# Kernel tuning notes

Hardware: AMD Instinct MI355X
Metric: run time of the kernel (lower is better)

Reference implementation:

```python
import jax, jax.numpy as jnp
import numpy as np

# config constants
D = 1024       # main_dim
HD = 64        # attn_head_dim
NH = 16        # attention heads = D // HD
H = 16         # main_head_num (routing heads)
KH = 8         # main_key_head_num
KC = 2         # main_key_repeat_num (KH*KC == H)
N = 128        # block_size
E = 4096       # total_layer_expert_num
RE = 4         # aux_router_expert_num
DE = 4         # selected experts per router
ET = RE * DE   # 16
B, S = 1, 2048
T = B * S
BC = T // N    # 16
EPS = 1e-5
THETA = 10000.0


def rmsnorm(x, w):
    return x * jax.lax.rsqrt(jnp.mean(x * x, axis=-1, keepdims=True) + EPS) * w


def l2norm(x):
    n = jnp.sqrt(jnp.sum(x * x, axis=-1, keepdims=True))
    return x / jnp.maximum(n, EPS)


def rope(x):
    # x: (b, h, s, a); matches RotaryEmb: y1 = x1*cos + x2*sin, y2 = -x1*sin + x2*cos
    a = x.shape[-1]
    s = x.shape[2]
    inv_freq = (1.0 / THETA) ** (jnp.arange(0, a, 2, dtype=jnp.float32) / a)
    freqs = jnp.arange(s, dtype=jnp.float32)[:, None] * inv_freq[None, :]  # (s, a/2)
    cos, sin = jnp.cos(freqs), jnp.sin(freqs)
    x1, x2 = jnp.split(x, 2, axis=-1)
    return jnp.concatenate([x1 * cos + x2 * sin, -x1 * sin + x2 * cos], axis=-1)


def setup_inputs() -> dict:
    key = jax.random.key(0)
    ks = jax.random.split(key, 10)
    return {
        "x_input": jax.random.normal(ks[0], (B, S, D), jnp.float32),
        "indices": jax.random.randint(ks[1], (BC, RE, DE), 0, E),
        "scores": jax.random.normal(ks[2], (T, ET, H), jnp.float32),
        "attn_w": jax.random.normal(ks[3], (D, 3 * D), jnp.float32) * 0.02,
        "attn_out_w": jax.random.normal(ks[4], (D, D), jnp.float32) * 0.02,
        "attn_norm_w": jnp.ones((D,), jnp.float32),
        "ffn_norm_w": jnp.ones((D,), jnp.float32),
        "ffn_experts": jax.random.normal(ks[5], (3, E, D, 1), jnp.float32) * 0.02,
        "keys": jax.random.normal(ks[6], (KH, D, E), jnp.float32) * 0.02,
        "head_probs": jnp.full((1, RE, E, H), 1.0 / H, jnp.float32)
                      + 0.01 * jax.random.normal(ks[7], (1, RE, E, H), jnp.float32),
        "score_probs": jnp.full((2, 1, RE, E, H), 0.5, jnp.float32)
                       + 0.01 * jax.random.normal(ks[8], (2, 1, RE, E, H), jnp.float32),
    }


def reference(x_input, indices, scores, attn_w, attn_out_w, attn_norm_w,
              ffn_norm_w, ffn_experts, keys, head_probs, score_probs):
    # --- attention block ---
    x = rmsnorm(x_input, attn_norm_w)
    qkv = x @ attn_w                                   # (b, s, 3d)
    xq, xk, xv = jnp.split(qkv, 3, axis=-1)

    def heads(t):  # 'b s (h a) -> b h s a'
        return t.reshape(B, S, NH, HD).transpose(0, 2, 1, 3)

    xq, xk, xv = heads(xq), heads(xk), heads(xv)
    xq, xk = l2norm(xq), l2norm(xk)                    # qk_norm
    xq, xk = rope(xq), rope(xk)

    att = jnp.einsum('bhqa,bhka->bhqk', xq, xk) / np.sqrt(HD)
    causal = jnp.tril(jnp.ones((S, S), bool))
    att = jnp.where(causal, att, -jnp.inf)
    att = jax.nn.softmax(att, axis=-1)
    x_attn = jnp.einsum('bhqk,bhka->bhqa', att, xv)
    x_attn = x_attn.transpose(0, 2, 1, 3).reshape(B, S, D)
    x_attn_output = x_attn @ attn_out_w
    x_ffn_input = x_attn_output + x_input

    # --- product-key routing ---
    x_ffn = rmsnorm(x_ffn_input, ffn_norm_w)
    xf = x_ffn.reshape(T, D)

    keys_r = jnp.repeat(keys, KC, axis=0)              # (H, D, E)
    ms = jnp.einsum('td,hde->teh', xf, keys_r)         # (T, E, H)

    idx_flat = indices.reshape(BC, ET)                 # (BC, ET)
    idx_tok = jnp.repeat(idx_flat, N, axis=0)          # (T, ET), token t -> block t//N
    main_g = jnp.take_along_axis(ms, idx_tok[:, :, None], axis=1)  # (T, ET, H)

    r_idx = jnp.arange(RE)[None, :, None]
    sp = score_probs[:, 0]                             # (2, RE, E, H)
    sp_g = sp[:, r_idx, indices]                       # (2, BC, RE, DE, H)
    sp_g = jnp.repeat(sp_g.reshape(2, BC, ET, H), N, axis=1)       # (2, T, ET, H)

    comb = jax.nn.sigmoid(sp_g[0] * main_g + sp_g[1] * scores)     # (T, ET, H)

    hp_g = head_probs[0][r_idx, indices]               # (BC, RE, DE, H)
    hp_g = jnp.repeat(hp_g.reshape(BC, ET, H), N, axis=0)          # (T, ET, H)

    w = jnp.sum(comb * hp_g, axis=-1)                  # (T, ET) pair weights

    # --- grouped GEMM over tiny (d -> expert_dim -> d) experts, SwiGLU ---
    Wg = ffn_experts[:, idx_tok]                       # (3, T, ET, D, expert_dim)
    h0 = jnp.einsum('td,tedk->tek', xf, Wg[0])
    h1 = jnp.einsum('td,tedk->tek', xf, Wg[1])
    act = jax.nn.silu(h0) * h1 * w[:, :, None]         # (T, ET, expert_dim)
    out = jnp.einsum('tek,tedk->td', act, Wg[2])       # sum over selected experts

    return out.reshape(B, S, D) + x_ffn_input
```

## Files before the change

### kernel.cpp

```cpp
#include <hip/hip_runtime.h>
#include <hip/hip_bf16.h>
#include <math.h>

#define D_   1024
#define HD_  64
#define NH_  16
#define H_   16
#define KH_  8
#define NT_  128
#define E_   4096
#define RE_  4
#define DE_  4
#define ET_  16
#define S_   2048
#define T_   2048
#define BC_  16
#define EPS_ 1e-5f

typedef short s16x8 __attribute__((ext_vector_type(8)));
typedef float f32x4 __attribute__((ext_vector_type(4)));

__device__ __forceinline__ unsigned short f2bf(float f) {
    union { float f; unsigned int u; } v; v.f = f;
    unsigned int r = (v.u + 0x7fffu + ((v.u >> 16) & 1u)) >> 16;
    return (unsigned short)r;
}
__device__ __forceinline__ float bf2f(unsigned short u) {
    union { unsigned int i; float f; } v;
    v.i = ((unsigned int)u) << 16;
    return v.f;
}

#define GLOAD16(gp, lp) __builtin_amdgcn_global_load_lds(                      \
    (__attribute__((address_space(1))) void*)(gp),                             \
    (__attribute__((address_space(3))) void*)(lp), 16, 0, 0)

__global__ __launch_bounds__(256) void rmsnorm_bf16_kernel(
    const float* __restrict__ x, const float* __restrict__ w,
    unsigned short* __restrict__ out)
{
    int row = blockIdx.x, tid = threadIdx.x;
    __shared__ float sred[4];
    float4 v = ((const float4*)(x + (size_t)row * D_))[tid];
    float ss = v.x*v.x + v.y*v.y + v.z*v.z + v.w*v.w;
#pragma unroll
    for (int off = 32; off > 0; off >>= 1) ss += __shfl_xor(ss, off);
    if ((tid & 63) == 0) sred[tid >> 6] = ss;
    __syncthreads();
    float tot = sred[0] + sred[1] + sred[2] + sred[3];
    float scale = rsqrtf(tot * (1.0f / D_) + EPS_);
    float4 wv = ((const float4*)w)[tid];
    ushort4 o;
    o.x = f2bf(v.x * scale * wv.x);
    o.y = f2bf(v.y * scale * wv.y);
    o.z = f2bf(v.z * scale * wv.z);
    o.w = f2bf(v.w * scale * wv.w);
    *(ushort4*)(out + (size_t)row * D_ + tid * 4) = o;
}

__global__ __launch_bounds__(256) void rmsnorm_dual_kernel(
    const float* __restrict__ x, const float* __restrict__ w,
    float* __restrict__ out, unsigned short* __restrict__ outb)
{
    int row = blockIdx.x, tid = threadIdx.x;
    __shared__ float sred[4];
    float4 v = ((const float4*)(x + (size_t)row * D_))[tid];
    float ss = v.x*v.x + v.y*v.y + v.z*v.z + v.w*v.w;
#pragma unroll
    for (int off = 32; off > 0; off >>= 1) ss += __shfl_xor(ss, off);
    if ((tid & 63) == 0) sred[tid >> 6] = ss;
    __syncthreads();
    float tot = sred[0] + sred[1] + sred[2] + sred[3];
    float scale = rsqrtf(tot * (1.0f / D_) + EPS_);
    float4 wv = ((const float4*)w)[tid];
    float4 o;
    o.x = v.x * scale * wv.x;
    o.y = v.y * scale * wv.y;
    o.z = v.z * scale * wv.z;
    o.w = v.w * scale * wv.w;
    ((float4*)(out + (size_t)row * D_))[tid] = o;
    ushort4 ob;
    ob.x = f2bf(o.x); ob.y = f2bf(o.y); ob.z = f2bf(o.z); ob.w = f2bf(o.w);
    *(ushort4*)(outb + (size_t)row * D_ + tid * 4) = ob;
}

__global__ __launch_bounds__(256) void convt_kernel(
    const float* __restrict__ src, unsigned short* __restrict__ dst,
    int R, int Ncols)
{
    __shared__ float tile[32][33];
    int bx = blockIdx.x * 32;
    int by = blockIdx.y * 32;
    int tx = threadIdx.x & 31, ty = threadIdx.x >> 5;
#pragma unroll
    for (int rr = 0; rr < 32; rr += 8)
        tile[ty + rr][tx] = src[(size_t)(by + ty + rr) * Ncols + bx + tx];
    __syncthreads();
#pragma unroll
    for (int rr = 0; rr < 32; rr += 8)
        dst[(size_t)(bx + ty + rr) * R + by + tx] = f2bf(tile[tx][ty + rr]);
}

__global__ __launch_bounds__(256) void transpose_v_kernel(
    const unsigned short* __restrict__ src, unsigned short* __restrict__ dst)
{
    __shared__ unsigned short tile[32][34];
    int h  = blockIdx.z;
    int d0 = blockIdx.x * 32;
    int s0 = blockIdx.y * 32;
    int tx = threadIdx.x & 31, ty = threadIdx.x >> 5;
    const unsigned short* sp = src + ((size_t)h * S_ + s0) * HD_ + d0;
#pragma unroll
    for (int rr = 0; rr < 32; rr += 8)
        tile[ty + rr][tx] = sp[(size_t)(ty + rr) * HD_ + tx];
    __syncthreads();
    unsigned short* dp = dst + ((size_t)h * HD_ + d0) * S_ + s0;
#pragma unroll
    for (int rr = 0; rr < 32; rr += 8)
        dp[(size_t)(ty + rr) * S_ + tx] = tile[tx][ty + rr];
}

template <int WITH_RES>
__global__ __launch_bounds__(256) void mfma_gemm_kernel(
    const unsigned short* __restrict__ A, const unsigned short* __restrict__ Bt,
    const float* __restrict__ res, float* __restrict__ C,
    int M, int N, int K)
{
    __shared__ __align__(16) short As[128][32];
    __shared__ __align__(16) short Bs[128][32];
    int tid = threadIdx.x;
    int wave = tid >> 6, lane = tid & 63;
    int ml = lane & 15, q = lane >> 4;
    int wr = wave >> 1, wc = wave & 1;
    int bm = blockIdx.y * 128, bn = blockIdx.x * 128;
    int srow = tid >> 2;
    int scol = (tid & 3) * 8;

    f32x4 acc[4][4];
#pragma unroll
    for (int i = 0; i < 4; i++)
#pragma unroll
        for (int j = 0; j < 4; j++) acc[i][j] = (f32x4){0.f, 0.f, 0.f, 0.f};

    const unsigned short* Ap = A  + (size_t)(bm + srow) * K + scol;
    const unsigned short* Bp = Bt + (size_t)(bn + srow) * K + scol;
    short* ldsA0 = &As[wave * 16][0];
    short* ldsA1 = &As[64 + wave * 16][0];
    short* ldsB0 = &Bs[wave * 16][0];
    short* ldsB1 = &Bs[64 + wave * 16][0];

    for (int k0 = 0; k0 < K; k0 += 32) {
        __syncthreads();
        GLOAD16(Ap + k0, ldsA0);
        GLOAD16(Ap + (size_t)64 * K + k0, ldsA1);
        GLOAD16(Bp + k0, ldsB0);
        GLOAD16(Bp + (size_t)64 * K + k0, ldsB1);
        __syncthreads();

        s16x8 af[4], bf[4];
#pragma unroll
        for (int i = 0; i < 4; i++)
            af[i] = *(const s16x8*)(&As[wr * 64 + i * 16 + ml][q * 8]);
#pragma unroll
        for (int j = 0; j < 4; j++)
            bf[j] = *(const s16x8*)(&Bs[wc * 64 + j * 16 + ml][q * 8]);
#pragma unroll
        for (int i = 0; i < 4; i++)
#pragma unroll
            for (int j = 0; j < 4; j++)
                acc[i][j] = __builtin_amdgcn_mfma_f32_16x16x32_bf16(
                    af[i], bf[j], acc[i][j], 0, 0, 0);
    }

#pragma unroll
    for (int i = 0; i < 4; i++) {
#pragma unroll
        for (int j = 0; j < 4; j++) {
            int col = bn + wc * 64 + j * 16 + ml;
#pragma unroll
            for (int r = 0; r < 4; r++) {
                int row = bm + wr * 64 + i * 16 + q * 4 + r;
                float v = acc[i][j][r];
                if (WITH_RES) v += res[(size_t)row * N + col];
                C[(size_t)row * N + col] = v;
            }
        }
    }
}

__global__ __launch_bounds__(256) void qkv_prep_kernel(
    const float* __restrict__ qkv, unsigned short* __restrict__ qh,
    unsigned short* __restrict__ khb, unsigned short* __restrict__ vhb)
{
    int pair = blockIdx.x * 4 + (threadIdx.x >> 6);
    int s = pair / NH_, h = pair % NH_;
    int lane = threadIdx.x & 63;

    size_t qoff = (size_t)s * (3 * D_) + h * HD_ + lane;
    float qv = qkv[qoff];
    float kv = qkv[qoff + D_];
    float vv = qkv[qoff + 2 * D_];

    float sq = qv * qv, sk = kv * kv;
#pragma unroll
    for (int off = 32; off > 0; off >>= 1) {
        sq += __shfl_xor(sq, off);
        sk += __shfl_xor(sk, off);
    }
    qv /= fmaxf(sqrtf(sq), EPS_);
    kv /= fmaxf(sqrtf(sk), EPS_);

    int j = lane & 31;
    float sign = (lane < 32) ? 1.0f : -1.0f;
    float inv_freq = exp2f((float)j * (-13.287712379549449f / 32.0f));
    float f = (float)s * inv_freq;
    float sn, cs;
    sincosf(f, &sn, &cs);
    float qo = __shfl_xor(qv, 32);
    float ko = __shfl_xor(kv, 32);
    qv = qv * cs + sign * qo * sn;
    kv = kv * cs + sign * ko * sn;

    size_t o = ((size_t)h * S_ + s) * HD_ + lane;
    qh[o]  = f2bf(qv * 0.125f);
    khb[o] = f2bf(kv);
    vhb[o] = f2bf(vv);
}

#define FS 72
__global__ __launch_bounds__(256) void flash_attn_mfma_kernel(
    const unsigned short* __restrict__ qh, const unsigned short* __restrict__ khb,
    const unsigned short* __restrict__ vhT, unsigned short* __restrict__ aob)
{
    __shared__ __align__(16) short Ks[2][64][FS];
    __shared__ __align__(16) short Vs[2][64][FS];
    __shared__ __align__(16) short Ps[4][16][FS];
    int u = blockIdx.x & 255;
    int v = blockIdx.x >> 8;
    int h = u & 15;
    int p = u >> 4;
    int t = v ? (31 - p) : p;
    int tid = threadIdx.x;
    int wq = tid >> 6;
    int lane = tid & 63;
    int ml = lane & 15, quad = lane >> 4;
    int srow = tid >> 2;
    int sc = (tid & 3) * 16;
    const unsigned short* Qb = qh  + (size_t)h * S_ * HD_;
    const unsigned short* Kb = khb + (size_t)h * S_ * HD_;
    const unsigned short* Vt = vhT + (size_t)h * HD_ * S_;

    int q0 = t * 64;
    int qrow = q0 + wq * 16 + ml;
    s16x8 aq0 = *(const s16x8*)(Qb + (size_t)qrow * HD_ + quad * 8);
    s16x8 aq1 = *(const s16x8*)(Qb + (size_t)qrow * HD_ + 32 + quad * 8);

    float m[4], l[4];
    f32x4 o[4];
#pragma unroll
    for (int r = 0; r < 4; r++) { m[r] = -INFINITY; l[r] = 0.f; }
#pragma unroll
    for (int nb = 0; nb < 4; nb++) o[nb] = (f32x4){0.f, 0.f, 0.f, 0.f};

    int4 kr0, kr1, vr0, vr1;
    {
        const unsigned short* kp = Kb + (size_t)srow * HD_ + sc;
        kr0 = *(const int4*)kp; kr1 = *(const int4*)(kp + 8);
        const unsigned short* vp = Vt + (size_t)srow * S_ + sc;
        vr0 = *(const int4*)vp; vr1 = *(const int4*)(vp + 8);
        *(int4*)(&Ks[0][srow][sc]) = kr0; *(int4*)(&Ks[0][srow][sc + 8]) = kr1;
        *(int4*)(&Vs[0][srow][sc]) = vr0; *(int4*)(&Vs[0][srow][sc + 8]) = vr1;
    }
    __syncthreads();
    int cur = 0;

    for (int kt = 0; kt <= t; kt++) {
        int k0 = kt * 64;
        if (kt < t) {
            const unsigned short* kp = Kb + (size_t)(k0 + 64 + srow) * HD_ + sc;
            kr0 = *(const int4*)kp; kr1 = *(const int4*)(kp + 8);
            const unsigned short* vp = Vt + (size_t)srow * S_ + k0 + 64 + sc;
            vr0 = *(const int4*)vp; vr1 = *(const int4*)(vp + 8);
        }

        f32x4 s[4];
#pragma unroll
        for (int nb = 0; nb < 4; nb++) s[nb] = (f32x4){0.f, 0.f, 0.f, 0.f};
        __builtin_amdgcn_s_setprio(1);
#pragma unroll
        for (int nb = 0; nb < 4; nb++) {
            s16x8 b0 = *(const s16x8*)(&Ks[cur][nb * 16 + ml][quad * 8]);
            s16x8 b1 = *(const s16x8*)(&Ks[cur][nb * 16 + ml][32 + quad * 8]);
            s[nb] = __builtin_amdgcn_mfma_f32_16x16x32_bf16(aq0, b0, s[nb], 0, 0, 0);
            s[nb] = __builtin_amdgcn_mfma_f32_16x16x32_bf16(aq1, b1, s[nb], 0, 0, 0);
        }
        __builtin_amdgcn_s_setprio(0);

        float sv[4][4];
#pragma unroll
        for (int nb = 0; nb < 4; nb++)
#pragma unroll
            for (int r = 0; r < 4; r++) {
                float val = s[nb][r];
                if (kt == t && (nb * 16 + ml) > (wq * 16 + quad * 4 + r))
                    val = -1e30f;
                sv[nb][r] = val;
            }
#pragma unroll
        for (int r = 0; r < 4; r++) {
            float rm = fmaxf(fmaxf(sv[0][r], sv[1][r]),
                             fmaxf(sv[2][r], sv[3][r]));
#pragma unroll
            for (int off = 1; off < 16; off <<= 1)
                rm = fmaxf(rm, __shfl_xor(rm, off));
            float mn = fmaxf(m[r], rm);
            float corr = __expf(m[r] - mn);
            m[r] = mn;
            float rs = 0.f;
#pragma unroll
            for (int nb = 0; nb < 4; nb++) {
                float pe = __expf(sv[nb][r] - mn);
                sv[nb][r] = pe;
                rs += pe;
            }
#pragma unroll
            for (int off = 1; off < 16; off <<= 1)
                rs += __shfl_xor(rs, off);
            l[r] = l[r] * corr + rs;
#pragma unroll
            for (int nb = 0; nb < 4; nb++) o[nb][r] *= corr;
        }

#pragma unroll
        for (int nb = 0; nb < 4; nb++)
#pragma unroll
            for (int r = 0; r < 4; r++)
                Ps[wq][quad * 4 + r][nb * 16 + ml] = (short)f2bf(sv[nb][r]);

        s16x8 ap0 = *(const s16x8*)(&Ps[wq][ml][quad * 8]);
        s16x8 ap1 = *(const s16x8*)(&Ps[wq][ml][32 + quad * 8]);
        __builtin_amdgcn_s_setprio(1);
#pragma unroll
        for (int nb = 0; nb < 4; nb++) {
            s16x8 b0 = *(const s16x8*)(&Vs[cur][nb * 16 + ml][quad * 8]);
            s16x8 b1 = *(const s16x8*)(&Vs[cur][nb * 16 + ml][32 + quad * 8]);
            o[nb] = __builtin_amdgcn_mfma_f32_16x16x32_bf16(ap0, b0, o[nb], 0, 0, 0);
            o[nb] = __builtin_amdgcn_mfma_f32_16x16x32_bf16(ap1, b1, o[nb], 0, 0, 0);
        }
        __builtin_amdgcn_s_setprio(0);

        __syncthreads();
        if (kt < t) {
            *(int4*)(&Ks[cur ^ 1][srow][sc])     = kr0;
            *(int4*)(&Ks[cur ^ 1][srow][sc + 8]) = kr1;
            *(int4*)(&Vs[cur ^ 1][srow][sc])     = vr0;
            *(int4*)(&Vs[cur ^ 1][srow][sc + 8]) = vr1;
            __syncthreads();
            cur ^= 1;
        }
    }

#pragma unroll
    for (int r = 0; r < 4; r++) {
        float inv = 1.0f / l[r];
        int row = q0 + wq * 16 + quad * 4 + r;
#pragma unroll
        for (int nb = 0; nb < 4; nb++)
            aob[(size_t)row * D_ + h * HD_ + nb * 16 + ml] =
                f2bf(o[nb][r] * inv);
    }
}

__global__ __launch_bounds__(256) void gather_keys_kernel(
    const float* __restrict__ keys, const int* __restrict__ indices,
    unsigned short* __restrict__ kgath)
{
    int bid = blockIdx.x;
    int pair = bid >> 3, kh = bid & 7;
    int idx = indices[pair];
    int tid = threadIdx.x;
    const float* kp = keys + (size_t)kh * D_ * E_ + idx;
    int d = tid * 4;
    ushort4 o;
    o.x = f2bf(kp[(size_t)(d + 0) * E_]);
    o.y = f2bf(kp[(size_t)(d + 1) * E_]);
    o.z = f2bf(kp[(size_t)(d + 2) * E_]);
    o.w = f2bf(kp[(size_t)(d + 3) * E_]);
    *(ushort4*)(kgath + ((size_t)pair * KH_ + kh) * D_ + d) = o;
}

__global__ __launch_bounds__(256) void score_gemm_kernel(
    const unsigned short* __restrict__ xfb, const unsigned short* __restrict__ kgath,
    float* __restrict__ msbufp)
{
    __shared__ __align__(16) short As[128][32];
    __shared__ __align__(16) short Bs[128][32];
    int c  = blockIdx.x >> 3;
    int sk = blockIdx.x & 7;
    const unsigned short* A  = xfb   + (size_t)c * 128 * D_ + sk * 128;
    const unsigned short* Bt = kgath + (size_t)c * 128 * D_ + sk * 128;
    int tid = threadIdx.x;
    int wave = tid >> 6, lane = tid & 63;
    int ml = lane & 15, q = lane >> 4;
    int wr = wave >> 1, wc = wave & 1;
    int srow = tid >> 2;
    int scol = (tid & 3) * 8;

    f32x4 acc[4][4];
#pragma unroll
    for (int i = 0; i < 4; i++)
#pragma unroll
        for (int j = 0; j < 4; j++) acc[i][j] = (f32x4){0.f, 0.f, 0.f, 0.f};

    const unsigned short* Ap = A  + (size_t)srow * D_ + scol;
    const unsigned short* Bp = Bt + (size_t)srow * D_ + scol;
    short* ldsA0 = &As[wave * 16][0];
    short* ldsA1 = &As[64 + wave * 16][0];
    short* ldsB0 = &Bs[wave * 16][0];
    short* ldsB1 = &Bs[64 + wave * 16][0];

    for (int k0 = 0; k0 < 128; k0 += 32) {
        __syncthreads();
        GLOAD16(Ap + k0, ldsA0);
        GLOAD16(Ap + (size_t)64 * D_ + k0, ldsA1);
        GLOAD16(Bp + k0, ldsB0);
        GLOAD16(Bp + (size_t)64 * D_ + k0, ldsB1);
        __syncthreads();

        s16x8 af[4], bf[4];
#pragma unroll
        for (int i = 0; i < 4; i++)
            af[i] = *(const s16x8*)(&As[wr * 64 + i * 16 + ml][q * 8]);
#pragma unroll
        for (int j = 0; j < 4; j++)
            bf[j] = *(const s16x8*)(&Bs[wc * 64 + j * 16 + ml][q * 8]);
#pragma unroll
        for (int i = 0; i < 4; i++)
#pragma unroll
            for (int j = 0; j < 4; j++)
                acc[i][j] = __builtin_amdgcn_mfma_f32_16x16x32_bf16(
                    af[i], bf[j], acc[i][j], 0, 0, 0);
    }

    float* out = msbufp + (size_t)blockIdx.x * 128 * 128;
#pragma unroll
    for (int i = 0; i < 4; i++)
#pragma unroll
        for (int j = 0; j < 4; j++) {
            int col = wc * 64 + j * 16 + ml;
#pragma unroll
            for (int r = 0; r < 4; r++) {
                int row = wr * 64 + i * 16 + q * 4 + r;
                out[(size_t)row * 128 + col] = acc[i][j][r];
            }
        }
}

__global__ __launch_bounds__(256) void gather_sp_kernel(
    const float* __restrict__ score_probs, const float* __restrict__ head_probs,
    const int* __restrict__ indices, float* __restrict__ spbuf)
{
    int c = blockIdx.x, tid = threadIdx.x;
    int e = tid >> 4, h = tid & 15;
    int idx = indices[c * ET_ + e];
    int r = e >> 2;
    float v0 = score_probs[((size_t)(0 * RE_ + r) * E_ + idx) * H_ + h];
    float v1 = score_probs[((size_t)(1 * RE_ + r) * E_ + idx) * H_ + h];
    float v2 = head_probs[((size_t)r * E_ + idx) * H_ + h];
    float* sp = spbuf + (size_t)c * 3 * 256;
    sp[tid] = v0;
    sp[256 + tid] = v1;
    sp[512 + tid] = v2;
}

__global__ __launch_bounds__(256) void moe_kernel(
    const float* __restrict__ xf, const float* __restrict__ xfi,
    const int* __restrict__ indices, const float* __restrict__ msbufp,
    const float* __restrict__ scores, const float* __restrict__ spbuf,
    const float* __restrict__ experts, float* __restrict__ out)
{
    int t = blockIdx.x, tid = threadIdx.x;
    int c = t >> 7;
    int trow = t & 127;
    __shared__ int sidx[ET_];
    __shared__ float sw[ET_];
    __shared__ float sact[ET_];
    __shared__ float sx[D_];
    if (tid < ET_) sidx[tid] = indices[c * ET_ + tid];
    float4 xv = ((const float4*)(xf + (size_t)t * D_))[tid];
    ((float4*)sx)[tid] = xv;
    {
        int e = tid >> 4, h = tid & 15;
        const float* mp = msbufp + ((size_t)(c * 8) * 128 + trow) * 128
                                 + e * 8 + (h >> 1);
        float ms = 0.f;
#pragma unroll
        for (int sck = 0; sck < 8; sck++) ms += mp[(size_t)sck * 128 * 128];
        float scv = scores[(size_t)t * (ET_ * H_) + tid];
        const float* sp = spbuf + (size_t)c * 3 * 256;
        float z = sp[tid] * ms + sp[256 + tid] * scv;
        float term = sp[512 + tid] / (1.0f + __expf(-z));
#pragma unroll
        for (int off = 1; off < 16; off <<= 1)
            term += __shfl_xor(term, off);
        if (h == 0) sw[e] = term;
    }
    __syncthreads();

    int wv = tid >> 6, lane = tid & 63;
#pragma unroll
    for (int ee = 0; ee < 4; ee++) {
        int e = wv * 4 + ee;
        int idx = sidx[e];
        size_t base = (size_t)idx * D_;
        float p0 = 0.f, p1 = 0.f;
#pragma unroll
        for (int rr = 0; rr < 4; rr++) {
            int dd = rr * 256 + lane * 4;
            float4 xr = *(const float4*)(sx + dd);
            float4 w0 = *(const float4*)(experts + base + dd);
            float4 w1 = *(const float4*)(experts + (size_t)E_ * D_ + base + dd);
            p0 += xr.x*w0.x + xr.y*w0.y + xr.z*w0.z + xr.w*w0.w;
            p1 += xr.x*w1.x + xr.y*w1.y + xr.z*w1.z + xr.w*w1.w;
        }
#pragma unroll
        for (int off = 32; off > 0; off >>= 1) {
            p0 += __shfl_xor(p0, off);
            p1 += __shfl_xor(p1, off);
        }
        if (lane == 0)
            sact[e] = p0 / (1.0f + __expf(-p0)) * p1 * sw[e];
    }
    __syncthreads();

    float a0 = 0.f, a1 = 0.f, a2 = 0.f, a3 = 0.f;
    const float* w2base = experts + (size_t)2 * E_ * D_;
#pragma unroll
    for (int e = 0; e < ET_; e++) {
        float act = sact[e];
        float4 w2 = *(const float4*)(w2base + (size_t)sidx[e] * D_ + tid * 4);
        a0 += act * w2.x;
        a1 += act * w2.y;
        a2 += act * w2.z;
        a3 += act * w2.w;
    }
    size_t o = (size_t)t * D_ + tid * 4;
    float4 rv = *(const float4*)(xfi + o);
    float4 ov;
    ov.x = a0 + rv.x;
    ov.y = a1 + rv.y;
    ov.z = a2 + rv.z;
    ov.w = a3 + rv.w;
    *(float4*)(out + o) = ov;
}

extern "C" void kernel_launch(void* const* d_in, const int* in_sizes, int n_in,
                              void* d_out, int out_size, void* d_ws, size_t ws_size,
                              hipStream_t stream)
{
    (void)in_sizes; (void)n_in; (void)out_size; (void)ws_size;
    const float* x_input     = (const float*)d_in[0];
    const int*   indices     = (const int*)d_in[1];
    const float* scores      = (const float*)d_in[2];
    const float* attn_w      = (const float*)d_in[3];
    const float* attn_out_w  = (const float*)d_in[4];
    const float* attn_norm_w = (const float*)d_in[5];
    const float* ffn_norm_w  = (const float*)d_in[6];
    const float* ffn_experts = (const float*)d_in[7];
    const float* keys        = (const float*)d_in[8];
    const float* head_probs  = (const float*)d_in[9];
    const float* score_probs = (const float*)d_in[10];
    float* out = (float*)d_out;

    float* ws = (float*)d_ws;
    const size_t MF = 1024 * 1024;
    float* qkv            = ws;
    unsigned short* aob   = (unsigned short*)ws;
    float* xfi            = ws + 1 * MF;
    float* xf             = ws + 3 * MF;
    unsigned short* woutT = (unsigned short*)(ws + 5 * MF);
    unsigned short* xnb   = (unsigned short*)(ws + 6 * MF);
    unsigned short* qh    = (unsigned short*)(ws + 6 * MF);
    unsigned short* xfb   = (unsigned short*)(ws + 6 * MF);
    unsigned short* wqkvT = (unsigned short*)(ws + 8 * MF);
    unsigned short* khb   = (unsigned short*)(ws + 8 * MF);
    unsigned short* vhb   = (unsigned short*)(ws + 10 * MF);
    unsigned short* kgath = (unsigned short*)(ws + 10 * MF);
    unsigned short* vhT   = (unsigned short*)(ws + 11 * MF);
    float* msbufp         = ws + 12 * MF;
    float* spbuf          = ws + 14 * MF;

    rmsnorm_bf16_kernel<<<T_, 256, 0, stream>>>(x_input, attn_norm_w, xnb);

    {
        dim3 g(3 * D_ / 32, D_ / 32);
        convt_kernel<<<g, 256, 0, stream>>>(attn_w, wqkvT, D_, 3 * D_);
    }

    {
        dim3 g(3 * D_ / 128, T_ / 128);
        mfma_gemm_kernel<0><<<g, 256, 0, stream>>>(xnb, wqkvT, nullptr, qkv,
                                                   T_, 3 * D_, D_);
    }

    qkv_prep_kernel<<<T_ * NH_ / 4, 256, 0, stream>>>(qkv, qh, khb, vhb);

    {
        dim3 g(HD_ / 32, S_ / 32, NH_);
        transpose_v_kernel<<<g, 256, 0, stream>>>(vhb, vhT);
    }

    flash_attn_mfma_kernel<<<(S_ / 64) * NH_, 256, 0, stream>>>(qh, khb, vhT, aob);

    {
        dim3 g(D_ / 32, D_ / 32);
        convt_kernel<<<g, 256, 0, stream>>>(attn_out_w, woutT, D_, D_);
    }

    {
        dim3 g(D_ / 128, T_ / 128);
        mfma_gemm_kernel<1><<<g, 256, 0, stream>>>(aob, woutT, x_input, xfi,
                                                   T_, D_, D_);
    }

    gather_keys_kernel<<<BC_ * ET_ * KH_, 256, 0, stream>>>(keys, indices, kgath);

    rmsnorm_dual_kernel<<<T_, 256, 0, stream>>>(xfi, ffn_norm_w, xf, xfb);

    score_gemm_kernel<<<BC_ * 8, 256, 0, stream>>>(xfb, kgath, msbufp);

    gather_sp_kernel<<<BC_, 256, 0, stream>>>(score_probs, head_probs,
                                              indices, spbuf);

    moe_kernel<<<T_, 256, 0, stream>>>(xf, xfi, indices, msbufp, scores, spbuf,
                                       ffn_experts, out);
}
```

Before: 410.6 us.

## Fuse preprocessing kernels and fold QKV l2norm/RoPE into GEMM epilogue

Merges the attention rmsnorm, both weight transpose-conversions and the key gather into one preprocess launch with block-range dispatch. It also writes QKV GEMM results straight to bf16 per-head buffers, applying l2norm and RoPE in the epilogue, which removes the fp32 qkv intermediate and the separate prep kernel. The score_probs and head_probs gather moves into the MoE kernel. The workspace layout is reshuffled to fit. This cuts launch count and intermediate memory traffic, at the cost of per-token redundant probability gathers and heavier epilogue shuffles and sincos calls.

```diff
diff --git a/kernel.cpp b/kernel.cpp
--- a/kernel.cpp
+++ b/kernel.cpp
@@ -25,37 +25,72 @@
     unsigned int r = (v.u + 0x7fffu + ((v.u >> 16) & 1u)) >> 16;
     return (unsigned short)r;
 }
-__device__ __forceinline__ float bf2f(unsigned short u) {
-    union { unsigned int i; float f; } v;
-    v.i = ((unsigned int)u) << 16;
-    return v.f;
-}
 
 #define GLOAD16(gp, lp) __builtin_amdgcn_global_load_lds(                      \
     (__attribute__((address_space(1))) void*)(gp),                             \
     (__attribute__((address_space(3))) void*)(lp), 16, 0, 0)
 
-__global__ __launch_bounds__(256) void rmsnorm_bf16_kernel(
-    const float* __restrict__ x, const float* __restrict__ w,
-    unsigned short* __restrict__ out)
-{
-    int row = blockIdx.x, tid = threadIdx.x;
+__global__ __launch_bounds__(256) void preprocess_kernel(
+    const float* __restrict__ x, const float* __restrict__ attn_norm_w,
+    unsigned short* __restrict__ xnb,
+    const float* __restrict__ attn_w, unsigned short* __restrict__ wqkvT,
+    const float* __restrict__ attn_out_w, unsigned short* __restrict__ woutT,
+    const float* __restrict__ keys, const int* __restrict__ indices,
+    unsigned short* __restrict__ kgath)
+{
+    __shared__ float tile[32][33];
     __shared__ float sred[4];
-    float4 v = ((const float4*)(x + (size_t)row * D_))[tid];
-    float ss = v.x*v.x + v.y*v.y + v.z*v.z + v.w*v.w;
-#pragma unroll
-    for (int off = 32; off > 0; off >>= 1) ss += __shfl_xor(ss, off);
-    if ((tid & 63) == 0) sred[tid >> 6] = ss;
-    __syncthreads();
-    float tot = sred[0] + sred[1] + sred[2] + sred[3];
-    float scale = rsqrtf(tot * (1.0f / D_) + EPS_);
-    float4 wv = ((const float4*)w)[tid];
-    ushort4 o;
-    o.x = f2bf(v.x * scale * wv.x);
-    o.y = f2bf(v.y * scale * wv.y);
-    o.z = f2bf(v.z * scale * wv.z);
-    o.w = f2bf(v.w * scale * wv.w);
-    *(ushort4*)(out + (size_t)row * D_ + tid * 4) = o;
+    int bid = blockIdx.x, tid = threadIdx.x;
+
+    if (bid < 2048) {
+        int row = bid;
+        float4 v = ((const float4*)(x + (size_t)row * D_))[tid];
+        float ss = v.x*v.x + v.y*v.y + v.z*v.z + v.w*v.w;
+#pragma unroll
+        for (int off = 32; off > 0; off >>= 1) ss += __shfl_xor(ss, off);
+        if ((tid & 63) == 0) sred[tid >> 6] = ss;
+        __syncthreads();
+        float tot = sred[0] + sred[1] + sred[2] + sred[3];
+        float scale = rsqrtf(tot * (1.0f / D_) + EPS_);
+        float4 wv = ((const float4*)attn_norm_w)[tid];
+        ushort4 o;
+        o.x = f2bf(v.x * scale * wv.x);
+        o.y = f2bf(v.y * scale * wv.y);
+        o.z = f2bf(v.z * scale * wv.z);
+        o.w = f2bf(v.w * scale * wv.w);
+        *(ushort4*)(xnb + (size_t)row * D_ + tid * 4) = o;
+    } else if (bid < 6144) {
+        const float* src; unsigned short* dst; int R, Ncols, bx, by;
+        if (bid < 5120) {
+            int cid = bid - 2048;
+            src = attn_w; dst = wqkvT; R = D_; Ncols = 3 * D_;
+            bx = (cid % 96) * 32; by = (cid / 96) * 32;
+        } else {
+            int cid = bid - 5120;
+            src = attn_out_w; dst = woutT; R = D_; Ncols = D_;
+            bx = (cid & 31) * 32; by = (cid >> 5) * 32;
+        }
+        int tx = tid & 31, ty = tid >> 5;
+#pragma unroll
+        for (int rr = 0; rr < 32; rr += 8)
+            tile[ty + rr][tx] = src[(size_t)(by + ty + rr) * Ncols + bx + tx];
+        __syncthreads();
+#pragma unroll
+        for (int rr = 0; rr < 32; rr += 8)
+            dst[(size_t)(bx + ty + rr) * R + by + tx] = f2bf(tile[tx][ty + rr]);
+    } else {
+        int gid = bid - 6144;
+        int pair = gid >> 3, kh = gid & 7;
+        int idx = indices[pair];
+        const float* kp = keys + (size_t)kh * D_ * E_ + idx;
+        int d = tid * 4;
+        ushort4 o;
+        o.x = f2bf(kp[(size_t)(d + 0) * E_]);
+        o.y = f2bf(kp[(size_t)(d + 1) * E_]);
+        o.z = f2bf(kp[(size_t)(d + 2) * E_]);
+        o.w = f2bf(kp[(size_t)(d + 3) * E_]);
+        *(ushort4*)(kgath + ((size_t)pair * KH_ + kh) * D_ + d) = o;
+    }
 }
 
 __global__ __launch_bounds__(256) void rmsnorm_dual_kernel(
@@ -84,23 +119,6 @@
     *(ushort4*)(outb + (size_t)row * D_ + tid * 4) = ob;
 }
 
-__global__ __launch_bounds__(256) void convt_kernel(
-    const float* __restrict__ src, unsigned short* __restrict__ dst,
-    int R, int Ncols)
-{
-    __shared__ float tile[32][33];
-    int bx = blockIdx.x * 32;
-    int by = blockIdx.y * 32;
-    int tx = threadIdx.x & 31, ty = threadIdx.x >> 5;
-#pragma unroll
-    for (int rr = 0; rr < 32; rr += 8)
-        tile[ty + rr][tx] = src[(size_t)(by + ty + rr) * Ncols + bx + tx];
-    __syncthreads();
-#pragma unroll
-    for (int rr = 0; rr < 32; rr += 8)
-        dst[(size_t)(bx + ty + rr) * R + by + tx] = f2bf(tile[tx][ty + rr]);
-}
-
 __global__ __launch_bounds__(256) void transpose_v_kernel(
     const unsigned short* __restrict__ src, unsigned short* __restrict__ dst)
 {
@@ -188,43 +206,95 @@
     }
 }
 
-__global__ __launch_bounds__(256) void qkv_prep_kernel(
-    const float* __restrict__ qkv, unsigned short* __restrict__ qh,
-    unsigned short* __restrict__ khb, unsigned short* __restrict__ vhb)
-{
-    int pair = blockIdx.x * 4 + (threadIdx.x >> 6);
-    int s = pair / NH_, h = pair % NH_;
-    int lane = threadIdx.x & 63;
-
-    size_t qoff = (size_t)s * (3 * D_) + h * HD_ + lane;
-    float qv = qkv[qoff];
-    float kv = qkv[qoff + D_];
-    float vv = qkv[qoff + 2 * D_];
-
-    float sq = qv * qv, sk = kv * kv;
-#pragma unroll
-    for (int off = 32; off > 0; off >>= 1) {
-        sq += __shfl_xor(sq, off);
-        sk += __shfl_xor(sk, off);
-    }
-    qv /= fmaxf(sqrtf(sq), EPS_);
-    kv /= fmaxf(sqrtf(sk), EPS_);
-
-    int j = lane & 31;
-    float sign = (lane < 32) ? 1.0f : -1.0f;
-    float inv_freq = exp2f((float)j * (-13.287712379549449f / 32.0f));
-    float f = (float)s * inv_freq;
-    float sn, cs;
-    sincosf(f, &sn, &cs);
-    float qo = __shfl_xor(qv, 32);
-    float ko = __shfl_xor(kv, 32);
-    qv = qv * cs + sign * qo * sn;
-    kv = kv * cs + sign * ko * sn;
-
-    size_t o = ((size_t)h * S_ + s) * HD_ + lane;
-    qh[o]  = f2bf(qv * 0.125f);
-    khb[o] = f2bf(kv);
-    vhb[o] = f2bf(vv);
+__global__ __launch_bounds__(256) void mfma_gemm_qkv_kernel(
+    const unsigned short* __restrict__ A, const unsigned short* __restrict__ Bt,
+    unsigned short* __restrict__ qh, unsigned short* __restrict__ khb,
+    unsigned short* __restrict__ vhb)
+{
+    const int K = D_;
+    __shared__ __align__(16) short As[128][32];
+    __shared__ __align__(16) short Bs[128][32];
+    int tid = threadIdx.x;
+    int wave = tid >> 6, lane = tid & 63;
+    int ml = lane & 15, q = lane >> 4;
+    int wr = wave >> 1, wc = wave & 1;
+    int bm = blockIdx.y * 128, bn = blockIdx.x * 128;
+    int srow = tid >> 2;
+    int scol = (tid & 3) * 8;
+
+    f32x4 acc[4][4];
+#pragma unroll
+    for (int i = 0; i < 4; i++)
+#pragma unroll
+        for (int j = 0; j < 4; j++) acc[i][j] = (f32x4){0.f, 0.f, 0.f, 0.f};
+
+    const unsigned short* Ap = A  + (size_t)(bm + srow) * K + scol;
+    const unsigned short* Bp = Bt + (size_t)(bn + srow) * K + scol;
+    short* ldsA0 = &As[wave * 16][0];
+    short* ldsA1 = &As[64 + wave * 16][0];
+    short* ldsB0 = &Bs[wave * 16][0];
+    short* ldsB1 = &Bs[64 + wave * 16][0];
+
+    for (int k0 = 0; k0 < K; k0 += 32) {
+        __syncthreads();
+        GLOAD16(Ap + k0, ldsA0);
+        GLOAD16(Ap + (size_t)64 * K + k0, ldsA1);
+        GLOAD16(Bp + k0, ldsB0);
+        GLOAD16(Bp + (size_t)64 * K + k0, ldsB1);
+        __syncthreads();
+
+        s16x8 af[4], bf[4];
+#pragma unroll
+        for (int i = 0; i < 4; i++)
+            af[i] = *(const s16x8*)(&As[wr * 64 + i * 16 + ml][q * 8]);
+#pragma unroll
+        for (int j = 0; j < 4; j++)
+            bf[j] = *(const s16x8*)(&Bs[wc * 64 + j * 16 + ml][q * 8]);
+#pragma unroll
+        for (int i = 0; i < 4; i++)
+#pragma unroll
+            for (int j = 0; j < 4; j++)
+                acc[i][j] = __builtin_amdgcn_mfma_f32_16x16x32_bf16(
+                    af[i], bf[j], acc[i][j], 0, 0, 0);
+    }
+
+    int sel = blockIdx.x >> 3;
+    int h = ((blockIdx.x & 7) << 1) + wc;
+    unsigned short* dst = (sel == 0) ? qh : (sel == 1) ? khb : vhb;
+    float qscale = (sel == 0) ? 0.125f : 1.0f;
+    float if0 = exp2f((float)ml * (-13.287712379549449f / 32.0f));
+    float if1 = exp2f((float)(16 + ml) * (-13.287712379549449f / 32.0f));
+
+#pragma unroll
+    for (int i = 0; i < 4; i++) {
+#pragma unroll
+        for (int r = 0; r < 4; r++) {
+            int row = bm + wr * 64 + i * 16 + q * 4 + r;
+            float v0 = acc[i][0][r], v1 = acc[i][1][r];
+            float v2 = acc[i][2][r], v3 = acc[i][3][r];
+            if (sel < 2) {
+                float ss = v0*v0 + v1*v1 + v2*v2 + v3*v3;
+#pragma unroll
+                for (int off = 1; off < 16; off <<= 1)
+                    ss += __shfl_xor(ss, off);
+                float inv = qscale / fmaxf(sqrtf(ss), EPS_);
+                v0 *= inv; v1 *= inv; v2 *= inv; v3 *= inv;
+                float sn0, cs0, sn1, cs1;
+                sincosf((float)row * if0, &sn0, &cs0);
+                sincosf((float)row * if1, &sn1, &cs1);
+                float o0 = v0 * cs0 + v2 * sn0;
+                float o2 = v2 * cs0 - v0 * sn0;
+                float o1 = v1 * cs1 + v3 * sn1;
+                float o3 = v3 * cs1 - v1 * sn1;
+                v0 = o0; v1 = o1; v2 = o2; v3 = o3;
+            }
+            size_t base = ((size_t)h * S_ + row) * HD_;
+            dst[base +      ml] = f2bf(v0);
+            dst[base + 16 + ml] = f2bf(v1);
+            dst[base + 32 + ml] = f2bf(v2);
+            dst[base + 48 + ml] = f2bf(v3);
+        }
+    }
 }
 
 #define FS 72
@@ -371,24 +441,6 @@
     }
 }
 
-__global__ __launch_bounds__(256) void gather_keys_kernel(
-    const float* __restrict__ keys, const int* __restrict__ indices,
-    unsigned short* __restrict__ kgath)
-{
-    int bid = blockIdx.x;
-    int pair = bid >> 3, kh = bid & 7;
-    int idx = indices[pair];
-    int tid = threadIdx.x;
-    const float* kp = keys + (size_t)kh * D_ * E_ + idx;
-    int d = tid * 4;
-    ushort4 o;
-    o.x = f2bf(kp[(size_t)(d + 0) * E_]);
-    o.y = f2bf(kp[(size_t)(d + 1) * E_]);
-    o.z = f2bf(kp[(size_t)(d + 2) * E_]);
-    o.w = f2bf(kp[(size_t)(d + 3) * E_]);
-    *(ushort4*)(kgath + ((size_t)pair * KH_ + kh) * D_ + d) = o;
-}
-
 __global__ __launch_bounds__(256) void score_gemm_kernel(
     const unsigned short* __restrict__ xfb, const unsigned short* __restrict__ kgath,
     float* __restrict__ msbufp)
@@ -456,27 +508,11 @@
         }
 }
 
-__global__ __launch_bounds__(256) void gather_sp_kernel(
-    const float* __restrict__ score_probs, const float* __restrict__ head_probs,
-    const int* __restrict__ indices, float* __restrict__ spbuf)
-{
-    int c = blockIdx.x, tid = threadIdx.x;
-    int e = tid >> 4, h = tid & 15;
-    int idx = indices[c * ET_ + e];
-    int r = e >> 2;
-    float v0 = score_probs[((size_t)(0 * RE_ + r) * E_ + idx) * H_ + h];
-    float v1 = score_probs[((size_t)(1 * RE_ + r) * E_ + idx) * H_ + h];
-    float v2 = head_probs[((size_t)r * E_ + idx) * H_ + h];
-    float* sp = spbuf + (size_t)c * 3 * 256;
-    sp[tid] = v0;
-    sp[256 + tid] = v1;
-    sp[512 + tid] = v2;
-}
-
 __global__ __launch_bounds__(256) void moe_kernel(
     const float* __restrict__ xf, const float* __restrict__ xfi,
     const int* __restrict__ indices, const float* __restrict__ msbufp,
-    const float* __restrict__ scores, const float* __restrict__ spbuf,
+    const float* __restrict__ scores,
+    const float* __restrict__ score_probs, const float* __restrict__ head_probs,
     const float* __restrict__ experts, float* __restrict__ out)
 {
     int t = blockIdx.x, tid = threadIdx.x;
@@ -490,20 +526,24 @@
     float4 xv = ((const float4*)(xf + (size_t)t * D_))[tid];
     ((float4*)sx)[tid] = xv;
     {
-        int e = tid >> 4, h = tid & 15;
+        int e = tid >> 4, hh = tid & 15;
+        int idx = indices[c * ET_ + e];
+        int rr = e >> 2;
         const float* mp = msbufp + ((size_t)(c * 8) * 128 + trow) * 128
-                                 + e * 8 + (h >> 1);
+                                 + e * 8 + (hh >> 1);
         float ms = 0.f;
 #pragma unroll
         for (int sck = 0; sck < 8; sck++) ms += mp[(size_t)sck * 128 * 128];
         float scv = scores[(size_t)t * (ET_ * H_) + tid];
-        const float* sp = spbuf + (size_t)c * 3 * 256;
-        float z = sp[tid] * ms + sp[256 + tid] * scv;
-        float term = sp[512 + tid] / (1.0f + __expf(-z));
+        float sp0 = score_probs[((size_t)rr * E_ + idx) * H_ + hh];
+        float sp1 = score_probs[((size_t)(RE_ + rr) * E_ + idx) * H_ + hh];
+        float hp  = head_probs[((size_t)rr * E_ + idx) * H_ + hh];
+        float z = sp0 * ms + sp1 * scv;
+        float term = hp / (1.0f + __expf(-z));
 #pragma unroll
         for (int off = 1; off < 16; off <<= 1)
             term += __shfl_xor(term, off);
-        if (h == 0) sw[e] = term;
+        if (hh == 0) sw[e] = term;
     }
     __syncthreads();
 
@@ -574,36 +614,28 @@
 
     float* ws = (float*)d_ws;
     const size_t MF = 1024 * 1024;
-    float* qkv            = ws;
-    unsigned short* aob   = (unsigned short*)ws;
-    float* xfi            = ws + 1 * MF;
-    float* xf             = ws + 3 * MF;
-    unsigned short* woutT = (unsigned short*)(ws + 5 * MF);
+    unsigned short* qh    = (unsigned short*)ws;
+    unsigned short* khb   = (unsigned short*)(ws + 1 * MF);
+    unsigned short* vhb   = (unsigned short*)(ws + 2 * MF);
+    unsigned short* vhT   = (unsigned short*)(ws + 3 * MF);
+    float* xfi            = ws + 4 * MF;
     unsigned short* xnb   = (unsigned short*)(ws + 6 * MF);
-    unsigned short* qh    = (unsigned short*)(ws + 6 * MF);
-    unsigned short* xfb   = (unsigned short*)(ws + 6 * MF);
+    unsigned short* aob   = (unsigned short*)(ws + 6 * MF);
+    unsigned short* woutT = (unsigned short*)(ws + 7 * MF);
     unsigned short* wqkvT = (unsigned short*)(ws + 8 * MF);
-    unsigned short* khb   = (unsigned short*)(ws + 8 * MF);
-    unsigned short* vhb   = (unsigned short*)(ws + 10 * MF);
+    float* xf             = ws + 8 * MF;
     unsigned short* kgath = (unsigned short*)(ws + 10 * MF);
-    unsigned short* vhT   = (unsigned short*)(ws + 11 * MF);
+    unsigned short* xfb   = (unsigned short*)(ws + 11 * MF);
     float* msbufp         = ws + 12 * MF;
-    float* spbuf          = ws + 14 * MF;
-
-    rmsnorm_bf16_kernel<<<T_, 256, 0, stream>>>(x_input, attn_norm_w, xnb);
-
-    {
-        dim3 g(3 * D_ / 32, D_ / 32);
-        convt_kernel<<<g, 256, 0, stream>>>(attn_w, wqkvT, D_, 3 * D_);
-    }
+
+    preprocess_kernel<<<8192, 256, 0, stream>>>(
+        x_input, attn_norm_w, xnb, attn_w, wqkvT, attn_out_w, woutT,
+        keys, indices, kgath);
 
     {
         dim3 g(3 * D_ / 128, T_ / 128);
-        mfma_gemm_kernel<0><<<g, 256, 0, stream>>>(xnb, wqkvT, nullptr, qkv,
-                                                   T_, 3 * D_, D_);
-    }
-
-    qkv_prep_kernel<<<T_ * NH_ / 4, 256, 0, stream>>>(qkv, qh, khb, vhb);
+        mfma_gemm_qkv_kernel<<<g, 256, 0, stream>>>(xnb, wqkvT, qh, khb, vhb);
+    }
 
     {
         dim3 g(HD_ / 32, S_ / 32, NH_);
@@ -611,11 +643,6 @@
     }
 
     flash_attn_mfma_kernel<<<(S_ / 64) * NH_, 256, 0, stream>>>(qh, khb, vhT, aob);
-
-    {
-        dim3 g(D_ / 32, D_ / 32);
-        convt_kernel<<<g, 256, 0, stream>>>(attn_out_w, woutT, D_, D_);
-    }
 
     {
         dim3 g(D_ / 128, T_ / 128);
@@ -623,15 +650,11 @@
                                                    T_, D_, D_);
     }
 
-    gather_keys_kernel<<<BC_ * ET_ * KH_, 256, 0, stream>>>(keys, indices, kgath);
-
     rmsnorm_dual_kernel<<<T_, 256, 0, stream>>>(xfi, ffn_norm_w, xf, xfb);
 
     score_gemm_kernel<<<BC_ * 8, 256, 0, stream>>>(xfb, kgath, msbufp);
 
-    gather_sp_kernel<<<BC_, 256, 0, stream>>>(score_probs, head_probs,
-                                              indices, spbuf);
-
-    moe_kernel<<<T_, 256, 0, stream>>>(xf, xfi, indices, msbufp, scores, spbuf,
+    moe_kernel<<<T_, 256, 0, stream>>>(xf, xfi, indices, msbufp, scores,
+                                       score_probs, head_probs,
                                        ffn_experts, out);
 }
```

After: 396.9 us. 3.3% less time.
